# Kernel tuning notes

Measured on AMD Instinct MI355X. Metric: run time of the kernel, lower is better.

The kernel has to match this reference:

```python
import jax, jax.numpy as jnp
import numpy as np
from jax import lax

N, T, H = 16, 2048, 512


def setup_inputs() -> dict:
    key = jax.random.key(0)
    ks = jax.random.split(key, 4)
    scale = 0.02  # keep gates/tanh out of hard saturation
    return {
        "x": jax.random.normal(ks[0], (N, T, H), dtype=jnp.float32),
        "hidden": jnp.zeros((N, H), dtype=jnp.float32),
        "Wq": jax.random.normal(ks[1], (H, 2 * H), dtype=jnp.float32) * scale,
        "bq": jnp.zeros((H,), dtype=jnp.float32),
        "Wk": jax.random.normal(ks[2], (H, 2 * H), dtype=jnp.float32) * scale,
        "bk": jnp.zeros((H,), dtype=jnp.float32),
        "Wv": jax.random.normal(ks[3], (H, 2 * H), dtype=jnp.float32) * scale,
        "bv": jnp.zeros((H,), dtype=jnp.float32),
    }


def reference(x, hidden, Wq, bq, Wk, bk, Wv, bv):
    # x: (N, T, H); hidden: (N, H). torch Linear: y = cat @ W.T + b
    def step(h, xt):
        cat = jnp.concatenate([xt, h], axis=-1)  # (N, 2H)
        q = cat @ Wq.T + bq
        k = cat @ Wk.T + bk
        v = cat @ Wv.T + bv
        w = jax.nn.sigmoid(q * k)
        h_new = (1.0 - w) * h + w * jnp.tanh(v)
        return h_new, h  # emit PRE-update hidden (matches torch append-before-update)

    xs = jnp.swapaxes(x, 0, 1)  # (T, N, H)
    h_final, hiddens = lax.scan(step, hidden, xs)
    return jnp.swapaxes(hiddens, 0, 1), h_final  # (N, T, H), (N, H)
```

## Files before the change

kernel.cpp:

```cpp
#include <hip/hip_runtime.h>

#define N_B 16
#define T_S 2048
#define H_D 512
#define TH_F ((size_t)T_S * H_D)
#define NTH ((size_t)N_B * TH_F)
#define NGROUP 8
#define WPG 32
#define THREADS 512
#define EXG 1024
#define EXP_W (NGROUP * EXG)

#define STASH(dst, src) asm volatile("v_accvgpr_write_b32 %0, %1" : "=a"(dst) : "v"(src))
#define FETCH(dst, src) asm volatile("v_accvgpr_read_b32 %0, %1" : "=v"(dst) : "a"(src))

__global__ __launch_bounds__(THREADS, 1) void rnn_persist(
    const float* __restrict__ x,
    const float* __restrict__ hidden,
    const float* __restrict__ Wq, const float* __restrict__ bq,
    const float* __restrict__ Wk, const float* __restrict__ bk,
    const float* __restrict__ Wv, const float* __restrict__ bv,
    float* __restrict__ out,
    unsigned long long* __restrict__ ex)
{
    const int tid  = threadIdx.x;
    const int lane = tid & 63;
    const int wv   = tid >> 6;
    const int g    = blockIdx.x & 7;
    const int wm   = blockIdx.x >> 3;
    const int b0 = 2 * g, b1 = 2 * g + 1;
    const int jA = wm * 16 + 2 * wv;

    __shared__ __align__(16) float hs[2][2][H_D];

    float awx[2][3][8], awh[2][3][8];
    #pragma unroll
    for (int r = 0; r < 2; ++r) {
        const int j = jA + r;
        #pragma unroll
        for (int m = 0; m < 3; ++m) {
            const float* W = (m == 0) ? Wq : (m == 1) ? Wk : Wv;
            const float* base = W + (size_t)j * 1024 + lane * 8;
            float4 x0 = *(const float4*)(base);
            float4 x1 = *(const float4*)(base + 4);
            float4 h0 = *(const float4*)(base + 512);
            float4 h1 = *(const float4*)(base + 516);
            STASH(awx[r][m][0], x0.x); STASH(awx[r][m][1], x0.y);
            STASH(awx[r][m][2], x0.z); STASH(awx[r][m][3], x0.w);
            STASH(awx[r][m][4], x1.x); STASH(awx[r][m][5], x1.y);
            STASH(awx[r][m][6], x1.z); STASH(awx[r][m][7], x1.w);
            STASH(awh[r][m][0], h0.x); STASH(awh[r][m][1], h0.y);
            STASH(awh[r][m][2], h0.z); STASH(awh[r][m][3], h0.w);
            STASH(awh[r][m][4], h1.x); STASH(awh[r][m][5], h1.y);
            STASH(awh[r][m][6], h1.z); STASH(awh[r][m][7], h1.w);
        }
    }

    const int jw = jA + ((lane >> 1) & 1);
    const int bw = (lane & 1) ? b1 : b0;
    const float bqw = bq[jw], bkw = bk[jw], bvw = bv[jw];
    float ho = hidden[bw * H_D + jw];

    const int h_nb  = tid >> 8;
    const int h_pos = (tid & 255) * 2;
    const int h_b   = h_nb ? b1 : b0;

    unsigned long long* const exg0 = ex + (size_t)g * EXG;
    unsigned long long* const exg1 = exg0 + EXP_W;
    unsigned long long* const sp0_p0 = exg0 + (size_t)tid * 2;
    unsigned long long* const sp0_p1 = exg1 + (size_t)tid * 2;
    const int exw_idx = (lane & 1) * 512 + jw;

    {
        float v0 = hidden[h_b * H_D + h_pos];
        float v1 = hidden[h_b * H_D + h_pos + 1];
        *(float2*)&hs[0][h_nb][h_pos] = make_float2(v0, v1);
        if (wm == 0) {
            out[(size_t)h_b * TH_F + h_pos]     = v0;
            out[(size_t)h_b * TH_F + h_pos + 1] = v1;
        }
    }
    __syncthreads();

    const float4* xb0 = (const float4*)(x + (size_t)b0 * TH_F) + lane * 2;
    const float4* xb1 = (const float4*)(x + (size_t)b1 * TH_F) + lane * 2;
    float ax[2][8];
    {
        float4 a = xb0[0], b = xb0[1], c = xb1[0], d = xb1[1];
        ax[0][0]=a.x; ax[0][1]=a.y; ax[0][2]=a.z; ax[0][3]=a.w;
        ax[0][4]=b.x; ax[0][5]=b.y; ax[0][6]=b.z; ax[0][7]=b.w;
        ax[1][0]=c.x; ax[1][1]=c.y; ax[1][2]=c.z; ax[1][3]=c.w;
        ax[1][4]=d.x; ax[1][5]=d.y; ax[1][6]=d.z; ax[1][7]=d.w;
    }

    for (int t = 0; t < T_S; ++t) {
        const bool do_next = (t + 1 < T_S);
        const int  p  = t & 1;
        unsigned long long* const spA = p ? sp0_p1 : sp0_p0;

        unsigned long long w0 = 0, w1 = 0;
        if (t > 0) {
            w0 = __hip_atomic_load(spA,     __ATOMIC_RELAXED, __HIP_MEMORY_SCOPE_AGENT);
            w1 = __hip_atomic_load(spA + 1, __ATOMIC_RELAXED, __HIP_MEMORY_SCOPE_AGENT);
        }

        float acc[2][3][2];
        #pragma unroll
        for (int r = 0; r < 2; ++r)
            #pragma unroll
            for (int m = 0; m < 3; ++m) {
                float wreg[8];
                #pragma unroll
                for (int c = 0; c < 8; ++c) FETCH(wreg[c], awx[r][m][c]);
                float s0 = 0.f, s1 = 0.f;
                #pragma unroll
                for (int c = 0; c < 8; ++c) {
                    s0 = fmaf(wreg[c], ax[0][c], s0);
                    s1 = fmaf(wreg[c], ax[1][c], s1);
                }
                acc[r][m][0] = s0; acc[r][m][1] = s1;
            }

        if (do_next) {
            const size_t o = (size_t)(t + 1) * 128;
            float4 a = xb0[o], b = xb0[o + 1], c = xb1[o], d = xb1[o + 1];
            ax[0][0]=a.x; ax[0][1]=a.y; ax[0][2]=a.z; ax[0][3]=a.w;
            ax[0][4]=b.x; ax[0][5]=b.y; ax[0][6]=b.z; ax[0][7]=b.w;
            ax[1][0]=c.x; ax[1][1]=c.y; ax[1][2]=c.z; ax[1][3]=c.w;
            ax[1][4]=d.x; ax[1][5]=d.y; ax[1][6]=d.z; ax[1][7]=d.w;
        }

        if (t > 0) {
            const unsigned tt = (unsigned)t;
            while ((((unsigned)(w0 >> 32)) != tt) |
                   (((unsigned)(w1 >> 32)) != tt)) {
                w0 = __hip_atomic_load(spA,     __ATOMIC_RELAXED, __HIP_MEMORY_SCOPE_AGENT);
                w1 = __hip_atomic_load(spA + 1, __ATOMIC_RELAXED, __HIP_MEMORY_SCOPE_AGENT);
            }
            union { unsigned u; float f; } c0, c1;
            c0.u = (unsigned)w0; c1.u = (unsigned)w1;
            *(float2*)&hs[p][h_nb][h_pos] = make_float2(c0.f, c1.f);
            __syncthreads();
        }

        float hbv[2][8];
        #pragma unroll
        for (int nb = 0; nb < 2; ++nb) {
            const float4* hp = (const float4*)&hs[p][nb][0] + lane * 2;
            float4 a0 = hp[0], a1 = hp[1];
            hbv[nb][0]=a0.x; hbv[nb][1]=a0.y; hbv[nb][2]=a0.z; hbv[nb][3]=a0.w;
            hbv[nb][4]=a1.x; hbv[nb][5]=a1.y; hbv[nb][6]=a1.z; hbv[nb][7]=a1.w;
        }
        #pragma unroll
        for (int r = 0; r < 2; ++r)
            #pragma unroll
            for (int m = 0; m < 3; ++m) {
                float wreg[8];
                #pragma unroll
                for (int c = 0; c < 8; ++c) FETCH(wreg[c], awh[r][m][c]);
                float s0 = acc[r][m][0], s1 = acc[r][m][1];
                #pragma unroll
                for (int c = 0; c < 8; ++c) {
                    s0 = fmaf(wreg[c], hbv[0][c], s0);
                    s1 = fmaf(wreg[c], hbv[1][c], s1);
                }
                acc[r][m][0] = s0; acc[r][m][1] = s1;
            }

        const bool lb0 = (lane & 1) != 0;
        const bool lb1 = (lane & 2) != 0;
        float a6[2][3];
        #pragma unroll
        for (int r = 0; r < 2; ++r)
            #pragma unroll
            for (int m = 0; m < 3; ++m) {
                float keep = lb0 ? acc[r][m][1] : acc[r][m][0];
                float send = lb0 ? acc[r][m][0] : acc[r][m][1];
                a6[r][m] = keep + __shfl_xor(send, 1);
            }
        float a3[3];
        #pragma unroll
        for (int m = 0; m < 3; ++m) {
            float keep = lb1 ? a6[1][m] : a6[0][m];
            float send = lb1 ? a6[0][m] : a6[1][m];
            a3[m] = keep + __shfl_xor(send, 2);
        }
        #pragma unroll
        for (int s = 4; s < 64; s <<= 1) {
            a3[0] += __shfl_xor(a3[0], s);
            a3[1] += __shfl_xor(a3[1], s);
            a3[2] += __shfl_xor(a3[2], s);
        }

        if (lane < 4) {
            const float q = a3[0] + bqw;
            const float k = a3[1] + bkw;
            const float v = a3[2] + bvw;
            const float e  = __expf(-q * k);
            const float w  = __builtin_amdgcn_rcpf(1.f + e);
            const float ev = __expf(2.f * v);
            const float th = 1.f - 2.f * __builtin_amdgcn_rcpf(ev + 1.f);
            const float hn = fmaf(w, th - ho, ho);
            if (do_next) {
                out[(size_t)bw * TH_F + (size_t)(t + 1) * H_D + jw] = hn;
                union { float f; unsigned u; } cv; cv.f = hn;
                unsigned long long* exwP = ((t + 1) & 1) ? (exg1 + exw_idx)
                                                         : (exg0 + exw_idx);
                __hip_atomic_store(exwP,
                    (((unsigned long long)(unsigned)(t + 1)) << 32) | cv.u,
                    __ATOMIC_RELAXED, __HIP_MEMORY_SCOPE_AGENT);
            } else {
                out[NTH + (size_t)bw * H_D + jw] = hn;
            }
            ho = hn;
        }
    }
}

extern "C" void kernel_launch(void* const* d_in, const int* in_sizes, int n_in,
                              void* d_out, int out_size, void* d_ws, size_t ws_size,
                              hipStream_t stream) {
    const float* x      = (const float*)d_in[0];
    const float* hidden = (const float*)d_in[1];
    const float* Wq     = (const float*)d_in[2];
    const float* bq     = (const float*)d_in[3];
    const float* Wk     = (const float*)d_in[4];
    const float* bk     = (const float*)d_in[5];
    const float* Wv     = (const float*)d_in[6];
    const float* bv     = (const float*)d_in[7];
    float* out = (float*)d_out;
    unsigned long long* ex = (unsigned long long*)d_ws;

    hipMemsetAsync(ex, 0, 2 * EXP_W * sizeof(unsigned long long), stream);

    void* args[] = { (void*)&x, (void*)&hidden,
                     (void*)&Wq, (void*)&bq, (void*)&Wk, (void*)&bk,
                     (void*)&Wv, (void*)&bv, (void*)&out, (void*)&ex };
    hipLaunchCooperativeKernel((const void*)rnn_persist,
                               dim3(NGROUP * WPG), dim3(THREADS),
                               args, 0, stream);
}
```

Measured before the change: 4.806 ms.

## Split two batch rows into staggered half-steps to overlap exchange latency

Each block now processes its two batch rows as separate half-steps within each timestep. Row A's hidden exchange and update run, then row B's, so the cross-block atomic wait for one row overlaps with compute on the other. Each row has its own poll, LDS fill and barrier, and the final reduction and gate math are done per row with fewer participating lanes. The cost is twice as many __syncthreads and reduction passes per step, and less FMA-level ILP because each weight fetch now serves one row instead of two.

After: 7.120 ms. 1.48x slower.

```diff
diff --git a/kernel.cpp b/kernel.cpp
--- a/kernel.cpp
+++ b/kernel.cpp
@@ -56,163 +56,220 @@
         }
     }
 
-    const int jw = jA + ((lane >> 1) & 1);
-    const int bw = (lane & 1) ? b1 : b0;
+    const int jw = jA + (lane & 1);
     const float bqw = bq[jw], bkw = bk[jw], bvw = bv[jw];
-    float ho = hidden[bw * H_D + jw];
-
-    const int h_nb  = tid >> 8;
-    const int h_pos = (tid & 255) * 2;
-    const int h_b   = h_nb ? b1 : b0;
+    float hoA = hidden[b0 * H_D + jw];
+    float hoB = hidden[b1 * H_D + jw];
 
     unsigned long long* const exg0 = ex + (size_t)g * EXG;
     unsigned long long* const exg1 = exg0 + EXP_W;
-    unsigned long long* const sp0_p0 = exg0 + (size_t)tid * 2;
-    unsigned long long* const sp0_p1 = exg1 + (size_t)tid * 2;
-    const int exw_idx = (lane & 1) * 512 + jw;
 
     {
-        float v0 = hidden[h_b * H_D + h_pos];
-        float v1 = hidden[h_b * H_D + h_pos + 1];
-        *(float2*)&hs[0][h_nb][h_pos] = make_float2(v0, v1);
+        float vA = hidden[b0 * H_D + tid];
+        float vB = hidden[b1 * H_D + tid];
+        hs[0][0][tid] = vA;
+        hs[0][1][tid] = vB;
         if (wm == 0) {
-            out[(size_t)h_b * TH_F + h_pos]     = v0;
-            out[(size_t)h_b * TH_F + h_pos + 1] = v1;
+            out[(size_t)b0 * TH_F + tid] = vA;
+            out[(size_t)b1 * TH_F + tid] = vB;
         }
     }
     __syncthreads();
 
-    const float4* xb0 = (const float4*)(x + (size_t)b0 * TH_F) + lane * 2;
-    const float4* xb1 = (const float4*)(x + (size_t)b1 * TH_F) + lane * 2;
-    float ax[2][8];
-    {
-        float4 a = xb0[0], b = xb0[1], c = xb1[0], d = xb1[1];
-        ax[0][0]=a.x; ax[0][1]=a.y; ax[0][2]=a.z; ax[0][3]=a.w;
-        ax[0][4]=b.x; ax[0][5]=b.y; ax[0][6]=b.z; ax[0][7]=b.w;
-        ax[1][0]=c.x; ax[1][1]=c.y; ax[1][2]=c.z; ax[1][3]=c.w;
-        ax[1][4]=d.x; ax[1][5]=d.y; ax[1][6]=d.z; ax[1][7]=d.w;
-    }
+    const float4* xpA = (const float4*)(x + (size_t)b0 * TH_F) + lane * 2;
+    const float4* xpB = (const float4*)(x + (size_t)b1 * TH_F) + lane * 2;
+    float4 xA0 = xpA[0], xA1 = xpA[1];
+    float4 xB0 = xpB[0], xB1 = xpB[1];
+
+    unsigned long long pwA = 0, pwB = 0;
 
     for (int t = 0; t < T_S; ++t) {
         const bool do_next = (t + 1 < T_S);
-        const int  p  = t & 1;
-        unsigned long long* const spA = p ? sp0_p1 : sp0_p0;
-
-        unsigned long long w0 = 0, w1 = 0;
-        if (t > 0) {
-            w0 = __hip_atomic_load(spA,     __ATOMIC_RELAXED, __HIP_MEMORY_SCOPE_AGENT);
-            w1 = __hip_atomic_load(spA + 1, __ATOMIC_RELAXED, __HIP_MEMORY_SCOPE_AGENT);
-        }
-
-        float acc[2][3][2];
+        const int  p = t & 1;
+        unsigned long long* const exgP  = p ? exg1 : exg0;
+        unsigned long long* const exgNP = p ? exg0 : exg1;
+
+        float acc[2][3];
         #pragma unroll
         for (int r = 0; r < 2; ++r)
             #pragma unroll
             for (int m = 0; m < 3; ++m) {
-                float wreg[8];
-                #pragma unroll
-                for (int c = 0; c < 8; ++c) FETCH(wreg[c], awx[r][m][c]);
-                float s0 = 0.f, s1 = 0.f;
-                #pragma unroll
-                for (int c = 0; c < 8; ++c) {
-                    s0 = fmaf(wreg[c], ax[0][c], s0);
-                    s1 = fmaf(wreg[c], ax[1][c], s1);
-                }
-                acc[r][m][0] = s0; acc[r][m][1] = s1;
-            }
-
+                float w0,w1,w2,w3,w4,w5,w6,w7;
+                FETCH(w0, awx[r][m][0]); FETCH(w1, awx[r][m][1]);
+                FETCH(w2, awx[r][m][2]); FETCH(w3, awx[r][m][3]);
+                FETCH(w4, awx[r][m][4]); FETCH(w5, awx[r][m][5]);
+                FETCH(w6, awx[r][m][6]); FETCH(w7, awx[r][m][7]);
+                float s = 0.f;
+                s = fmaf(w0, xA0.x, s); s = fmaf(w1, xA0.y, s);
+                s = fmaf(w2, xA0.z, s); s = fmaf(w3, xA0.w, s);
+                s = fmaf(w4, xA1.x, s); s = fmaf(w5, xA1.y, s);
+                s = fmaf(w6, xA1.z, s); s = fmaf(w7, xA1.w, s);
+                acc[r][m] = s;
+            }
         if (do_next) {
             const size_t o = (size_t)(t + 1) * 128;
-            float4 a = xb0[o], b = xb0[o + 1], c = xb1[o], d = xb1[o + 1];
-            ax[0][0]=a.x; ax[0][1]=a.y; ax[0][2]=a.z; ax[0][3]=a.w;
-            ax[0][4]=b.x; ax[0][5]=b.y; ax[0][6]=b.z; ax[0][7]=b.w;
-            ax[1][0]=c.x; ax[1][1]=c.y; ax[1][2]=c.z; ax[1][3]=c.w;
-            ax[1][4]=d.x; ax[1][5]=d.y; ax[1][6]=d.z; ax[1][7]=d.w;
-        }
-
+            xA0 = xpA[o]; xA1 = xpA[o + 1];
+        }
         if (t > 0) {
             const unsigned tt = (unsigned)t;
-            while ((((unsigned)(w0 >> 32)) != tt) |
-                   (((unsigned)(w1 >> 32)) != tt)) {
-                w0 = __hip_atomic_load(spA,     __ATOMIC_RELAXED, __HIP_MEMORY_SCOPE_AGENT);
-                w1 = __hip_atomic_load(spA + 1, __ATOMIC_RELAXED, __HIP_MEMORY_SCOPE_AGENT);
-            }
-            union { unsigned u; float f; } c0, c1;
-            c0.u = (unsigned)w0; c1.u = (unsigned)w1;
-            *(float2*)&hs[p][h_nb][h_pos] = make_float2(c0.f, c1.f);
+            while ((unsigned)(pwA >> 32) != tt)
+                pwA = __hip_atomic_load(exgP + tid, __ATOMIC_RELAXED,
+                                        __HIP_MEMORY_SCOPE_AGENT);
+            union { unsigned u; float f; } cv; cv.u = (unsigned)pwA;
+            hs[p][0][tid] = cv.f;
             __syncthreads();
         }
-
-        float hbv[2][8];
-        #pragma unroll
-        for (int nb = 0; nb < 2; ++nb) {
-            const float4* hp = (const float4*)&hs[p][nb][0] + lane * 2;
-            float4 a0 = hp[0], a1 = hp[1];
-            hbv[nb][0]=a0.x; hbv[nb][1]=a0.y; hbv[nb][2]=a0.z; hbv[nb][3]=a0.w;
-            hbv[nb][4]=a1.x; hbv[nb][5]=a1.y; hbv[nb][6]=a1.z; hbv[nb][7]=a1.w;
-        }
+        {
+            const float4* hp = (const float4*)&hs[p][0][0] + lane * 2;
+            const float4 h0v = hp[0], h1v = hp[1];
+            #pragma unroll
+            for (int r = 0; r < 2; ++r)
+                #pragma unroll
+                for (int m = 0; m < 3; ++m) {
+                    float w0,w1,w2,w3,w4,w5,w6,w7;
+                    FETCH(w0, awh[r][m][0]); FETCH(w1, awh[r][m][1]);
+                    FETCH(w2, awh[r][m][2]); FETCH(w3, awh[r][m][3]);
+                    FETCH(w4, awh[r][m][4]); FETCH(w5, awh[r][m][5]);
+                    FETCH(w6, awh[r][m][6]); FETCH(w7, awh[r][m][7]);
+                    float s = acc[r][m];
+                    s = fmaf(w0, h0v.x, s); s = fmaf(w1, h0v.y, s);
+                    s = fmaf(w2, h0v.z, s); s = fmaf(w3, h0v.w, s);
+                    s = fmaf(w4, h1v.x, s); s = fmaf(w5, h1v.y, s);
+                    s = fmaf(w6, h1v.z, s); s = fmaf(w7, h1v.w, s);
+                    acc[r][m] = s;
+                }
+        }
+        {
+            float a3[3];
+            const bool rs = (lane & 1) != 0;
+            #pragma unroll
+            for (int m = 0; m < 3; ++m) {
+                float keep = rs ? acc[1][m] : acc[0][m];
+                float send = rs ? acc[0][m] : acc[1][m];
+                a3[m] = keep + __shfl_xor(send, 1);
+            }
+            #pragma unroll
+            for (int s = 2; s < 64; s <<= 1) {
+                a3[0] += __shfl_xor(a3[0], s);
+                a3[1] += __shfl_xor(a3[1], s);
+                a3[2] += __shfl_xor(a3[2], s);
+            }
+            if (lane < 2) {
+                const float q = a3[0] + bqw;
+                const float k = a3[1] + bkw;
+                const float v = a3[2] + bvw;
+                const float e  = __expf(-q * k);
+                const float w  = __builtin_amdgcn_rcpf(1.f + e);
+                const float ev = __expf(2.f * v);
+                const float th = 1.f - 2.f * __builtin_amdgcn_rcpf(ev + 1.f);
+                const float hn = fmaf(w, th - hoA, hoA);
+                if (do_next) {
+                    out[(size_t)b0 * TH_F + (size_t)(t + 1) * H_D + jw] = hn;
+                    union { float f; unsigned u; } cw; cw.f = hn;
+                    __hip_atomic_store(exgNP + jw,
+                        (((unsigned long long)(unsigned)(t + 1)) << 32) | cw.u,
+                        __ATOMIC_RELAXED, __HIP_MEMORY_SCOPE_AGENT);
+                } else {
+                    out[NTH + (size_t)b0 * H_D + jw] = hn;
+                }
+                hoA = hn;
+            }
+        }
+        if (t > 0) {
+            pwB = __hip_atomic_load(exgP + 512 + tid, __ATOMIC_RELAXED,
+                                    __HIP_MEMORY_SCOPE_AGENT);
+            asm volatile("" ::: "memory");
+        }
+
         #pragma unroll
         for (int r = 0; r < 2; ++r)
             #pragma unroll
             for (int m = 0; m < 3; ++m) {
-                float wreg[8];
+                float w0,w1,w2,w3,w4,w5,w6,w7;
+                FETCH(w0, awx[r][m][0]); FETCH(w1, awx[r][m][1]);
+                FETCH(w2, awx[r][m][2]); FETCH(w3, awx[r][m][3]);
+                FETCH(w4, awx[r][m][4]); FETCH(w5, awx[r][m][5]);
+                FETCH(w6, awx[r][m][6]); FETCH(w7, awx[r][m][7]);
+                float s = 0.f;
+                s = fmaf(w0, xB0.x, s); s = fmaf(w1, xB0.y, s);
+                s = fmaf(w2, xB0.z, s); s = fmaf(w3, xB0.w, s);
+                s = fmaf(w4, xB1.x, s); s = fmaf(w5, xB1.y, s);
+                s = fmaf(w6, xB1.z, s); s = fmaf(w7, xB1.w, s);
+                acc[r][m] = s;
+            }
+        if (do_next) {
+            const size_t o = (size_t)(t + 1) * 128;
+            xB0 = xpB[o]; xB1 = xpB[o + 1];
+        }
+        if (t > 0) {
+            const unsigned tt = (unsigned)t;
+            while ((unsigned)(pwB >> 32) != tt)
+                pwB = __hip_atomic_load(exgP + 512 + tid, __ATOMIC_RELAXED,
+                                        __HIP_MEMORY_SCOPE_AGENT);
+            union { unsigned u; float f; } cv; cv.u = (unsigned)pwB;
+            hs[p][1][tid] = cv.f;
+            __syncthreads();
+        }
+        {
+            const float4* hp = (const float4*)&hs[p][1][0] + lane * 2;
+            const float4 h0v = hp[0], h1v = hp[1];
+            #pragma unroll
+            for (int r = 0; r < 2; ++r)
                 #pragma unroll
-                for (int c = 0; c < 8; ++c) FETCH(wreg[c], awh[r][m][c]);
-                float s0 = acc[r][m][0], s1 = acc[r][m][1];
-                #pragma unroll
-                for (int c = 0; c < 8; ++c) {
-                    s0 = fmaf(wreg[c], hbv[0][c], s0);
-                    s1 = fmaf(wreg[c], hbv[1][c], s1);
-                }
-                acc[r][m][0] = s0; acc[r][m][1] = s1;
-            }
-
-        const bool lb0 = (lane & 1) != 0;
-        const bool lb1 = (lane & 2) != 0;
-        float a6[2][3];
-        #pragma unroll
-        for (int r = 0; r < 2; ++r)
-            #pragma unroll
-            for (int m = 0; m < 3; ++m) {
-                float keep = lb0 ? acc[r][m][1] : acc[r][m][0];
-                float send = lb0 ? acc[r][m][0] : acc[r][m][1];
-                a6[r][m] = keep + __shfl_xor(send, 1);
-            }
-        float a3[3];
-        #pragma unroll
-        for (int m = 0; m < 3; ++m) {
-            float keep = lb1 ? a6[1][m] : a6[0][m];
-            float send = lb1 ? a6[0][m] : a6[1][m];
-            a3[m] = keep + __shfl_xor(send, 2);
-        }
-        #pragma unroll
-        for (int s = 4; s < 64; s <<= 1) {
-            a3[0] += __shfl_xor(a3[0], s);
-            a3[1] += __shfl_xor(a3[1], s);
-            a3[2] += __shfl_xor(a3[2], s);
-        }
-
-        if (lane < 4) {
-            const float q = a3[0] + bqw;
-            const float k = a3[1] + bkw;
-            const float v = a3[2] + bvw;
-            const float e  = __expf(-q * k);
-            const float w  = __builtin_amdgcn_rcpf(1.f + e);
-            const float ev = __expf(2.f * v);
-            const float th = 1.f - 2.f * __builtin_amdgcn_rcpf(ev + 1.f);
-            const float hn = fmaf(w, th - ho, ho);
-            if (do_next) {
-                out[(size_t)bw * TH_F + (size_t)(t + 1) * H_D + jw] = hn;
-                union { float f; unsigned u; } cv; cv.f = hn;
-                unsigned long long* exwP = ((t + 1) & 1) ? (exg1 + exw_idx)
-                                                         : (exg0 + exw_idx);
-                __hip_atomic_store(exwP,
-                    (((unsigned long long)(unsigned)(t + 1)) << 32) | cv.u,
-                    __ATOMIC_RELAXED, __HIP_MEMORY_SCOPE_AGENT);
-            } else {
-                out[NTH + (size_t)bw * H_D + jw] = hn;
-            }
-            ho = hn;
+                for (int m = 0; m < 3; ++m) {
+                    float w0,w1,w2,w3,w4,w5,w6,w7;
+                    FETCH(w0, awh[r][m][0]); FETCH(w1, awh[r][m][1]);
+                    FETCH(w2, awh[r][m][2]); FETCH(w3, awh[r][m][3]);
+                    FETCH(w4, awh[r][m][4]); FETCH(w5, awh[r][m][5]);
+                    FETCH(w6, awh[r][m][6]); FETCH(w7, awh[r][m][7]);
+                    float s = acc[r][m];
+                    s = fmaf(w0, h0v.x, s); s = fmaf(w1, h0v.y, s);
+                    s = fmaf(w2, h0v.z, s); s = fmaf(w3, h0v.w, s);
+                    s = fmaf(w4, h1v.x, s); s = fmaf(w5, h1v.y, s);
+                    s = fmaf(w6, h1v.z, s); s = fmaf(w7, h1v.w, s);
+                    acc[r][m] = s;
+                }
+        }
+        {
+            float a3[3];
+            const bool rs = (lane & 1) != 0;
+            #pragma unroll
+            for (int m = 0; m < 3; ++m) {
+                float keep = rs ? acc[1][m] : acc[0][m];
+                float send = rs ? acc[0][m] : acc[1][m];
+                a3[m] = keep + __shfl_xor(send, 1);
+            }
+            #pragma unroll
+            for (int s = 2; s < 64; s <<= 1) {
+                a3[0] += __shfl_xor(a3[0], s);
+                a3[1] += __shfl_xor(a3[1], s);
+                a3[2] += __shfl_xor(a3[2], s);
+            }
+            if (lane < 2) {
+                const float q = a3[0] + bqw;
+                const float k = a3[1] + bkw;
+                const float v = a3[2] + bvw;
+                const float e  = __expf(-q * k);
+                const float w  = __builtin_amdgcn_rcpf(1.f + e);
+                const float ev = __expf(2.f * v);
+                const float th = 1.f - 2.f * __builtin_amdgcn_rcpf(ev + 1.f);
+                const float hn = fmaf(w, th - hoB, hoB);
+                if (do_next) {
+                    out[(size_t)b1 * TH_F + (size_t)(t + 1) * H_D + jw] = hn;
+                    union { float f; unsigned u; } cw; cw.f = hn;
+                    __hip_atomic_store(exgNP + 512 + jw,
+                        (((unsigned long long)(unsigned)(t + 1)) << 32) | cw.u,
+                        __ATOMIC_RELAXED, __HIP_MEMORY_SCOPE_AGENT);
+                } else {
+                    out[NTH + (size_t)b1 * H_D + jw] = hn;
+                }
+                hoB = hn;
+            }
+        }
+        if (do_next) {
+            pwA = __hip_atomic_load(exgNP + tid, __ATOMIC_RELAXED,
+                                    __HIP_MEMORY_SCOPE_AGENT);
+            asm volatile("" ::: "memory");
         }
     }
 }
```

## Use fp16 packed dot2 for matvecs and exchange hidden state as fp16 pairs

Applied to the files above, without the earlier changes.

Weights are packed into fp16 pairs in accumulation registers, and x and the hidden state are converted to fp16 so that each step's matvec uses dot2 instructions. That halves the weight register footprint and the FMA count. The cross-block hidden exchange now packs two fp16 hidden values (batch pair) into one 64-bit flagged word, so each thread polls one word instead of two. The cost is reduced precision in the recurrent state over 2048 steps, which may drift from the fp32 reference.

New measurement: 6.700 ms. 1.39x slower.

```diff
diff --git a/kernel.cpp b/kernel.cpp
--- a/kernel.cpp
+++ b/kernel.cpp
@@ -8,11 +8,20 @@
 #define NGROUP 8
 #define WPG 32
 #define THREADS 512
-#define EXG 1024
-#define EXP_W (NGROUP * EXG)
-
-#define STASH(dst, src) asm volatile("v_accvgpr_write_b32 %0, %1" : "=a"(dst) : "v"(src))
-#define FETCH(dst, src) asm volatile("v_accvgpr_read_b32 %0, %1" : "=v"(dst) : "a"(src))
+#define PLANE_W (NGROUP * H_D)
+
+typedef __fp16 f16x2 __attribute__((ext_vector_type(2)));
+union UH { unsigned u; f16x2 h; };
+union US { unsigned short s; __fp16 f; };
+
+#define STASHU(dst, src) asm volatile("v_accvgpr_write_b32 %0, %1" : "=a"(dst) : "v"(src))
+#define FETCHU(dst, src) asm volatile("v_accvgpr_read_b32 %0, %1" : "=v"(dst) : "a"(src))
+
+#if __has_builtin(__builtin_amdgcn_fdot2)
+#define DOT2(a, b, c) __builtin_amdgcn_fdot2((a), (b), (c), false)
+#else
+#define DOT2(a, b, c) fmaf((float)(a).x, (float)(b).x, fmaf((float)(a).y, (float)(b).y, (c)))
+#endif
 
 __global__ __launch_bounds__(THREADS, 1) void rnn_persist(
     const float* __restrict__ x,
@@ -31,9 +40,9 @@
     const int b0 = 2 * g, b1 = 2 * g + 1;
     const int jA = wm * 16 + 2 * wv;
 
-    __shared__ __align__(16) float hs[2][2][H_D];
-
-    float awx[2][3][8], awh[2][3][8];
+    __shared__ __align__(16) __fp16 hs[2][2][H_D];
+
+    unsigned awx[2][3][4], awh[2][3][4];
     #pragma unroll
     for (int r = 0; r < 2; ++r) {
         const int j = jA + r;
@@ -45,14 +54,15 @@
             float4 x1 = *(const float4*)(base + 4);
             float4 h0 = *(const float4*)(base + 512);
             float4 h1 = *(const float4*)(base + 516);
-            STASH(awx[r][m][0], x0.x); STASH(awx[r][m][1], x0.y);
-            STASH(awx[r][m][2], x0.z); STASH(awx[r][m][3], x0.w);
-            STASH(awx[r][m][4], x1.x); STASH(awx[r][m][5], x1.y);
-            STASH(awx[r][m][6], x1.z); STASH(awx[r][m][7], x1.w);
-            STASH(awh[r][m][0], h0.x); STASH(awh[r][m][1], h0.y);
-            STASH(awh[r][m][2], h0.z); STASH(awh[r][m][3], h0.w);
-            STASH(awh[r][m][4], h1.x); STASH(awh[r][m][5], h1.y);
-            STASH(awh[r][m][6], h1.z); STASH(awh[r][m][7], h1.w);
+            UH p;
+            p.h = __builtin_amdgcn_cvt_pkrtz(x0.x, x0.y); STASHU(awx[r][m][0], p.u);
+            p.h = __builtin_amdgcn_cvt_pkrtz(x0.z, x0.w); STASHU(awx[r][m][1], p.u);
+            p.h = __builtin_amdgcn_cvt_pkrtz(x1.x, x1.y); STASHU(awx[r][m][2], p.u);
+            p.h = __builtin_amdgcn_cvt_pkrtz(x1.z, x1.w); STASHU(awx[r][m][3], p.u);
+            p.h = __builtin_amdgcn_cvt_pkrtz(h0.x, h0.y); STASHU(awh[r][m][0], p.u);
+            p.h = __builtin_amdgcn_cvt_pkrtz(h0.z, h0.w); STASHU(awh[r][m][1], p.u);
+            p.h = __builtin_amdgcn_cvt_pkrtz(h1.x, h1.y); STASHU(awh[r][m][2], p.u);
+            p.h = __builtin_amdgcn_cvt_pkrtz(h1.z, h1.w); STASHU(awh[r][m][3], p.u);
         }
     }
 
@@ -61,109 +71,95 @@
     const float bqw = bq[jw], bkw = bk[jw], bvw = bv[jw];
     float ho = hidden[bw * H_D + jw];
 
-    const int h_nb  = tid >> 8;
-    const int h_pos = (tid & 255) * 2;
-    const int h_b   = h_nb ? b1 : b0;
-
-    unsigned long long* const exg0 = ex + (size_t)g * EXG;
-    unsigned long long* const exg1 = exg0 + EXP_W;
-    unsigned long long* const sp0_p0 = exg0 + (size_t)tid * 2;
-    unsigned long long* const sp0_p1 = exg1 + (size_t)tid * 2;
-    const int exw_idx = (lane & 1) * 512 + jw;
-
     {
-        float v0 = hidden[h_b * H_D + h_pos];
-        float v1 = hidden[h_b * H_D + h_pos + 1];
-        *(float2*)&hs[0][h_nb][h_pos] = make_float2(v0, v1);
+        float hA = hidden[b0 * H_D + tid];
+        float hB = hidden[b1 * H_D + tid];
+        hs[0][0][tid] = (__fp16)hA;
+        hs[0][1][tid] = (__fp16)hB;
         if (wm == 0) {
-            out[(size_t)h_b * TH_F + h_pos]     = v0;
-            out[(size_t)h_b * TH_F + h_pos + 1] = v1;
+            out[(size_t)b0 * TH_F + tid] = hA;
+            out[(size_t)b1 * TH_F + tid] = hB;
         }
     }
     __syncthreads();
 
-    const float4* xb0 = (const float4*)(x + (size_t)b0 * TH_F) + lane * 2;
-    const float4* xb1 = (const float4*)(x + (size_t)b1 * TH_F) + lane * 2;
-    float ax[2][8];
-    {
-        float4 a = xb0[0], b = xb0[1], c = xb1[0], d = xb1[1];
-        ax[0][0]=a.x; ax[0][1]=a.y; ax[0][2]=a.z; ax[0][3]=a.w;
-        ax[0][4]=b.x; ax[0][5]=b.y; ax[0][6]=b.z; ax[0][7]=b.w;
-        ax[1][0]=c.x; ax[1][1]=c.y; ax[1][2]=c.z; ax[1][3]=c.w;
-        ax[1][4]=d.x; ax[1][5]=d.y; ax[1][6]=d.z; ax[1][7]=d.w;
-    }
+    const float4* xpA = (const float4*)(x + (size_t)b0 * TH_F) + lane * 2;
+    const float4* xpB = (const float4*)(x + (size_t)b1 * TH_F) + lane * 2;
+    float4 xA0 = xpA[0], xA1 = xpA[1];
+    float4 xB0 = xpB[0], xB1 = xpB[1];
 
     for (int t = 0; t < T_S; ++t) {
         const bool do_next = (t + 1 < T_S);
-        const int  p  = t & 1;
-        unsigned long long* const spA = p ? sp0_p1 : sp0_p0;
-
-        unsigned long long w0 = 0, w1 = 0;
+        const int  p = t & 1;
+        unsigned long long* const spin = ex + (size_t)p * PLANE_W + g * H_D + tid;
+
+        unsigned long long w = 0;
         if (t > 0) {
-            w0 = __hip_atomic_load(spA,     __ATOMIC_RELAXED, __HIP_MEMORY_SCOPE_AGENT);
-            w1 = __hip_atomic_load(spA + 1, __ATOMIC_RELAXED, __HIP_MEMORY_SCOPE_AGENT);
-        }
+            w = __hip_atomic_load(spin, __ATOMIC_RELAXED, __HIP_MEMORY_SCOPE_AGENT);
+            asm volatile("" ::: "memory");
+        }
+
+        UH xk[2][4];
+        xk[0][0].h = __builtin_amdgcn_cvt_pkrtz(xA0.x, xA0.y);
+        xk[0][1].h = __builtin_amdgcn_cvt_pkrtz(xA0.z, xA0.w);
+        xk[0][2].h = __builtin_amdgcn_cvt_pkrtz(xA1.x, xA1.y);
+        xk[0][3].h = __builtin_amdgcn_cvt_pkrtz(xA1.z, xA1.w);
+        xk[1][0].h = __builtin_amdgcn_cvt_pkrtz(xB0.x, xB0.y);
+        xk[1][1].h = __builtin_amdgcn_cvt_pkrtz(xB0.z, xB0.w);
+        xk[1][2].h = __builtin_amdgcn_cvt_pkrtz(xB1.x, xB1.y);
+        xk[1][3].h = __builtin_amdgcn_cvt_pkrtz(xB1.z, xB1.w);
 
         float acc[2][3][2];
         #pragma unroll
         for (int r = 0; r < 2; ++r)
             #pragma unroll
             for (int m = 0; m < 3; ++m) {
-                float wreg[8];
-                #pragma unroll
-                for (int c = 0; c < 8; ++c) FETCH(wreg[c], awx[r][m][c]);
+                UH w0, w1, w2, w3;
+                FETCHU(w0.u, awx[r][m][0]); FETCHU(w1.u, awx[r][m][1]);
+                FETCHU(w2.u, awx[r][m][2]); FETCHU(w3.u, awx[r][m][3]);
                 float s0 = 0.f, s1 = 0.f;
-                #pragma unroll
-                for (int c = 0; c < 8; ++c) {
-                    s0 = fmaf(wreg[c], ax[0][c], s0);
-                    s1 = fmaf(wreg[c], ax[1][c], s1);
-                }
+                s0 = DOT2(w0.h, xk[0][0].h, s0); s1 = DOT2(w0.h, xk[1][0].h, s1);
+                s0 = DOT2(w1.h, xk[0][1].h, s0); s1 = DOT2(w1.h, xk[1][1].h, s1);
+                s0 = DOT2(w2.h, xk[0][2].h, s0); s1 = DOT2(w2.h, xk[1][2].h, s1);
+                s0 = DOT2(w3.h, xk[0][3].h, s0); s1 = DOT2(w3.h, xk[1][3].h, s1);
                 acc[r][m][0] = s0; acc[r][m][1] = s1;
             }
 
         if (do_next) {
             const size_t o = (size_t)(t + 1) * 128;
-            float4 a = xb0[o], b = xb0[o + 1], c = xb1[o], d = xb1[o + 1];
-            ax[0][0]=a.x; ax[0][1]=a.y; ax[0][2]=a.z; ax[0][3]=a.w;
-            ax[0][4]=b.x; ax[0][5]=b.y; ax[0][6]=b.z; ax[0][7]=b.w;
-            ax[1][0]=c.x; ax[1][1]=c.y; ax[1][2]=c.z; ax[1][3]=c.w;
-            ax[1][4]=d.x; ax[1][5]=d.y; ax[1][6]=d.z; ax[1][7]=d.w;
+            xA0 = xpA[o]; xA1 = xpA[o + 1];
+            xB0 = xpB[o]; xB1 = xpB[o + 1];
         }
 
         if (t > 0) {
             const unsigned tt = (unsigned)t;
-            while ((((unsigned)(w0 >> 32)) != tt) |
-                   (((unsigned)(w1 >> 32)) != tt)) {
-                w0 = __hip_atomic_load(spA,     __ATOMIC_RELAXED, __HIP_MEMORY_SCOPE_AGENT);
-                w1 = __hip_atomic_load(spA + 1, __ATOMIC_RELAXED, __HIP_MEMORY_SCOPE_AGENT);
-            }
-            union { unsigned u; float f; } c0, c1;
-            c0.u = (unsigned)w0; c1.u = (unsigned)w1;
-            *(float2*)&hs[p][h_nb][h_pos] = make_float2(c0.f, c1.f);
+            while ((unsigned)(w >> 32) != tt)
+                w = __hip_atomic_load(spin, __ATOMIC_RELAXED, __HIP_MEMORY_SCOPE_AGENT);
+            US lo, hi;
+            lo.s = (unsigned short)(w & 0xFFFFu);
+            hi.s = (unsigned short)((w >> 16) & 0xFFFFu);
+            hs[p][0][tid] = lo.f;
+            hs[p][1][tid] = hi.f;
             __syncthreads();
         }
 
-        float hbv[2][8];
-        #pragma unroll
-        for (int nb = 0; nb < 2; ++nb) {
-            const float4* hp = (const float4*)&hs[p][nb][0] + lane * 2;
-            float4 a0 = hp[0], a1 = hp[1];
-            hbv[nb][0]=a0.x; hbv[nb][1]=a0.y; hbv[nb][2]=a0.z; hbv[nb][3]=a0.w;
-            hbv[nb][4]=a1.x; hbv[nb][5]=a1.y; hbv[nb][6]=a1.z; hbv[nb][7]=a1.w;
-        }
+        uint4 hA4 = ((const uint4*)&hs[p][0][0])[lane];
+        uint4 hB4 = ((const uint4*)&hs[p][1][0])[lane];
+        UH hk[2][4];
+        hk[0][0].u = hA4.x; hk[0][1].u = hA4.y; hk[0][2].u = hA4.z; hk[0][3].u = hA4.w;
+        hk[1][0].u = hB4.x; hk[1][1].u = hB4.y; hk[1][2].u = hB4.z; hk[1][3].u = hB4.w;
         #pragma unroll
         for (int r = 0; r < 2; ++r)
             #pragma unroll
             for (int m = 0; m < 3; ++m) {
-                float wreg[8];
-                #pragma unroll
-                for (int c = 0; c < 8; ++c) FETCH(wreg[c], awh[r][m][c]);
+                UH w0, w1, w2, w3;
+                FETCHU(w0.u, awh[r][m][0]); FETCHU(w1.u, awh[r][m][1]);
+                FETCHU(w2.u, awh[r][m][2]); FETCHU(w3.u, awh[r][m][3]);
                 float s0 = acc[r][m][0], s1 = acc[r][m][1];
-                #pragma unroll
-                for (int c = 0; c < 8; ++c) {
-                    s0 = fmaf(wreg[c], hbv[0][c], s0);
-                    s1 = fmaf(wreg[c], hbv[1][c], s1);
-                }
+                s0 = DOT2(w0.h, hk[0][0].h, s0); s1 = DOT2(w0.h, hk[1][0].h, s1);
+                s0 = DOT2(w1.h, hk[0][1].h, s0); s1 = DOT2(w1.h, hk[1][1].h, s1);
+                s0 = DOT2(w2.h, hk[0][2].h, s0); s1 = DOT2(w2.h, hk[1][2].h, s1);
+                s0 = DOT2(w3.h, hk[0][3].h, s0); s1 = DOT2(w3.h, hk[1][3].h, s1);
                 acc[r][m][0] = s0; acc[r][m][1] = s1;
             }
 
@@ -197,18 +193,22 @@
             const float k = a3[1] + bkw;
             const float v = a3[2] + bvw;
             const float e  = __expf(-q * k);
-            const float w  = __builtin_amdgcn_rcpf(1.f + e);
+            const float wg = __builtin_amdgcn_rcpf(1.f + e);
             const float ev = __expf(2.f * v);
             const float th = 1.f - 2.f * __builtin_amdgcn_rcpf(ev + 1.f);
-            const float hn = fmaf(w, th - ho, ho);
+            const float hn = fmaf(wg, th - ho, ho);
             if (do_next) {
                 out[(size_t)bw * TH_F + (size_t)(t + 1) * H_D + jw] = hn;
-                union { float f; unsigned u; } cv; cv.f = hn;
-                unsigned long long* exwP = ((t + 1) & 1) ? (exg1 + exw_idx)
-                                                         : (exg0 + exw_idx);
-                __hip_atomic_store(exwP,
-                    (((unsigned long long)(unsigned)(t + 1)) << 32) | cv.u,
-                    __ATOMIC_RELAXED, __HIP_MEMORY_SCOPE_AGENT);
+                US h16; h16.f = (__fp16)hn;
+                const int partner = __shfl_xor((int)h16.s, 1);
+                if ((lane & 1) == 0) {
+                    const unsigned long long word =
+                        (((unsigned long long)(unsigned)(t + 1)) << 32)
+                        | (unsigned)h16.s
+                        | (((unsigned)partner & 0xFFFFu) << 16);
+                    __hip_atomic_store(ex + (size_t)((t + 1) & 1) * PLANE_W + g * H_D + jw,
+                                       word, __ATOMIC_RELAXED, __HIP_MEMORY_SCOPE_AGENT);
+                }
             } else {
                 out[NTH + (size_t)bw * H_D + jw] = hn;
             }
@@ -231,12 +231,12 @@
     float* out = (float*)d_out;
     unsigned long long* ex = (unsigned long long*)d_ws;
 
-    hipMemsetAsync(ex, 0, 2 * EXP_W * sizeof(unsigned long long), stream);
+    (void)hipMemsetAsync(ex, 0, 2 * PLANE_W * sizeof(unsigned long long), stream);
 
     void* args[] = { (void*)&x, (void*)&hidden,
                      (void*)&Wq, (void*)&bq, (void*)&Wk, (void*)&bk,
                      (void*)&Wv, (void*)&bv, (void*)&out, (void*)&ex };
-    hipLaunchCooperativeKernel((const void*)rnn_persist,
-                               dim3(NGROUP * WPG), dim3(THREADS),
-                               args, 0, stream);
+    (void)hipLaunchCooperativeKernel((const void*)rnn_persist,
+                                     dim3(NGROUP * WPG), dim3(THREADS),
+                                     args, 0, stream);
 }
```
